# Performance work log

Measured on AMD Instinct MI355X. Metric: run time of the kernel, lower is better.

## Reference

```python
import jax, jax.numpy as jnp
import numpy as np

B, LA, LQ, LO, H, OUT = 32, 2048, 64, 32, 1024, 5


def _kaiming(key, out_f, in_f):
    return jax.random.normal(key, (out_f, in_f), jnp.float32) * np.sqrt(2.0 / in_f)


def setup_inputs() -> dict:
    key = jax.random.key(0)
    ks = jax.random.split(key, 16)
    inp = {
        "article_contexts": jax.random.normal(ks[0], (B, LA, H), jnp.float32),
        "question_contexts": jax.random.normal(ks[1], (B, LQ, H), jnp.float32),
        "options_embeds": jax.random.normal(ks[2], (B, 5, LO, H), jnp.float32),
        "answer_indices": jax.random.randint(ks[3], (B,), 0, LQ),
    }
    # mlp_att (article-question attention) params
    inp["a_Qw"], inp["a_Qb"] = _kaiming(ks[4], H, H), jnp.zeros((H,), jnp.float32)
    inp["a_Kw"], inp["a_Kb"] = _kaiming(ks[5], H, H), jnp.zeros((H,), jnp.float32)
    inp["a_Vw"], inp["a_Vb"] = _kaiming(ks[6], H, H), jnp.zeros((H,), jnp.float32)
    inp["a_vw"], inp["a_vb"] = _kaiming(ks[7], 1, H), jnp.zeros((1,), jnp.float32)
    # dot_layer (option attention) params
    inp["d_Qw"], inp["d_Qb"] = _kaiming(ks[8], H, H), jnp.zeros((H,), jnp.float32)
    inp["d_Kw"], inp["d_Kb"] = _kaiming(ks[9], H, H), jnp.zeros((H,), jnp.float32)
    inp["d_Vw"], inp["d_Vb"] = _kaiming(ks[10], H, H), jnp.zeros((H,), jnp.float32)
    inp["d_vw"], inp["d_vb"] = _kaiming(ks[11], 1, H), jnp.zeros((1,), jnp.float32)
    # final linear: hidden_size*5 -> output_dim
    inp["f_w"], inp["f_b"] = _kaiming(ks[12], OUT, 5 * H), jnp.zeros((OUT,), jnp.float32)
    return inp


def _mlp_att(Q, K, V, Qw, Qb, Kw, Kb, Vw, Vb, vw, vb):
    # Q: [B, H]; K, V: [B, (..opt..), L, H]. Dropout is identity (eval mode).
    Qp = Q @ Qw.T + Qb                      # [B, H]
    Kp = K @ Kw.T + Kb                      # [..., L, H]
    Vp = V @ Vw.T + Vb                      # [..., L, H]
    while Qp.ndim < Kp.ndim:
        Qp = Qp[..., None, :]
    M = jnp.tanh(Qp + Kp)                   # [..., L, H]
    scores = jax.nn.softmax(M @ vw.T + vb, axis=-2)  # softmax over L, [..., L, 1]
    return jnp.sum(Vp * scores, axis=-2)    # [..., H]


def reference(article_contexts, question_contexts, options_embeds, answer_indices,
              a_Qw, a_Qb, a_Kw, a_Kb, a_Vw, a_Vb, a_vw, a_vb,
              d_Qw, d_Qb, d_Kw, d_Kb, d_Vw, d_Vb, d_vw, d_vb,
              f_w, f_b):
    b = article_contexts.shape[0]
    # gather question context at the answer index -> [B, H]
    oqc = question_contexts[jnp.arange(b), answer_indices]
    # article-question additive attention -> [B, H]
    aq = _mlp_att(oqc, article_contexts, article_contexts,
                  a_Qw, a_Qb, a_Kw, a_Kb, a_Vw, a_Vb, a_vw, a_vb)
    # per-option additive attention, vectorized over the 5 options -> [B, 5, H]
    feats = _mlp_att(aq, options_embeds, options_embeds,
                     d_Qw, d_Qb, d_Kw, d_Kb, d_Vw, d_Vb, d_vw, d_vb)
    # concat options along feature dim, final linear -> [B, OUT]
    logits = feats.reshape(b, -1) @ f_w.T + f_b
    return logits
```

## Files before the change

### kernel.cpp

```cpp
#include <hip/hip_runtime.h>
#include <hip/hip_bf16.h>
#include <math.h>

#define HDIM 1024
#define NB 32
#define LA 2048
#define LO 32

typedef __attribute__((ext_vector_type(8))) short bf16x8;
typedef __attribute__((ext_vector_type(4))) float f32x4;
typedef unsigned int u32;

__device__ __forceinline__ float tanh_fast(float x){
    return 2.0f / (1.0f + __expf(-2.0f * x)) - 1.0f;
}

__device__ __forceinline__ void load_lds16(const void* gptr, void* lptr){
    __builtin_amdgcn_global_load_lds(
        (const __attribute__((address_space(1))) u32*)gptr,
        (__attribute__((address_space(3))) u32*)lptr, 16, 0, 0);
}

__global__ void zero_kernel(float* __restrict__ p, int n){
    int i = blockIdx.x * blockDim.x + threadIdx.x;
    int stride = gridDim.x * blockDim.x;
    for (; i < n; i += stride) p[i] = 0.0f;
}

__global__ void conv_bf16_kernel(const float* __restrict__ in, __hip_bfloat16* __restrict__ out, long n){
    long i = ((long)blockIdx.x * blockDim.x + threadIdx.x) * 4;
    long stride = (long)gridDim.x * blockDim.x * 4;
    for (; i < n; i += stride){
        float4 v = *(const float4*)(in + i);
        union { __hip_bfloat16 h[4]; short4 s; } u;
        u.h[0] = __float2bfloat16(v.x); u.h[1] = __float2bfloat16(v.y);
        u.h[2] = __float2bfloat16(v.z); u.h[3] = __float2bfloat16(v.w);
        *(short4*)(out + i) = u.s;
    }
}

__global__ void gather_kernel(const float* __restrict__ qc, const int* __restrict__ ans,
                              float* __restrict__ oqc){
    int b = blockIdx.x, tid = threadIdx.x;
    int idx = ans[b];
    const float* src = qc + ((size_t)b * 64 + idx) * HDIM;
    float* dst = oqc + (size_t)b * HDIM;
    #pragma unroll
    for (int l = 0; l < 4; l++) dst[tid + l * 256] = src[tid + l * 256];
}

__global__ __launch_bounds__(256) void proj_kernel(
    const float* __restrict__ in, const float* __restrict__ W,
    const float* __restrict__ bias, float* __restrict__ out){
    __shared__ float xin[HDIM];
    const int g = blockIdx.x, tid = threadIdx.x;
    const int lane = tid & 63, wave = tid >> 6;
    *(float4*)&xin[tid * 4] = *(const float4*)&in[(size_t)g * HDIM + tid * 4];
    __syncthreads();
    float4 xv[4];
    #pragma unroll
    for (int c = 0; c < 4; c++) xv[c] = *(const float4*)&xin[(c * 64 + lane) * 4];
    const int hbase = blockIdx.y * 64 + wave * 16;
    #pragma unroll 4
    for (int r = 0; r < 16; r++){
        int h = hbase + r;
        const float* Wr = W + (size_t)h * HDIM;
        float p = 0.f;
        #pragma unroll
        for (int c = 0; c < 4; c++){
            float4 wv = *(const float4*)&Wr[(c * 64 + lane) * 4];
            p = fmaf(xv[c].x, wv.x, p); p = fmaf(xv[c].y, wv.y, p);
            p = fmaf(xv[c].z, wv.z, p); p = fmaf(xv[c].w, wv.w, p);
        }
        #pragma unroll
        for (int off = 1; off < 64; off <<= 1) p += __shfl_xor(p, off, 64);
        if (lane == 0) out[(size_t)g * HDIM + h] = p + bias[h];
    }
}

__global__ __launch_bounds__(512, 2) void score_mfma8p(
    const __hip_bfloat16* __restrict__ X, const __hip_bfloat16* __restrict__ Kw,
    const float* __restrict__ Kb, const float* __restrict__ Qp,
    const float* __restrict__ vw, float* __restrict__ s,
    int row_off, int rows_per_batch)
{
    __shared__ __align__(16) char lds[131072];
    const int tid = threadIdx.x;
    const int lane = tid & 63, wid = tid >> 6;
    const int wm = wid >> 2, wn = wid & 3;
    const int lr = lane & 15, lg = lane >> 4;

    const int na = gridDim.x >> 2;
    const int bid = blockIdx.x;
    const int xcd = bid & 7, seq = bid >> 3;
    const int a_idx = xcd * (na >> 3) + (seq >> 2);
    const int h_idx = seq & 3;
    const int a0 = a_idx * 256, h0 = h_idx * 256;

    f32x4 acc[8][4] = {};
    bf16x8 av[8], bv[4];

    const int rA = tid >> 2;
    const int csw = ((tid & 3) * 16) ^ (((rA >> 1) & 3) << 4);
    const char* pA = (const char*)Kw + (size_t)(h0 + rA) * 2048 + csw;
    const char* pB = (const char*)X  + (size_t)(a0 + rA) * 2048 + csw;
    char* dst0 = lds + tid * 16;

    int aoff[8], boff[4];
    #pragma unroll
    for (int hf = 0; hf < 8; hf++){
        int rw = wm * 128 + hf * 16 + lr;
        aoff[hf] = rw * 64 + ((lg * 16) ^ (((rw >> 1) & 3) << 4));
    }
    #pragma unroll
    for (int af = 0; af < 4; af++){
        int rw = wn * 64 + af * 16 + lr;
        boff[af] = 16384 + rw * 64 + ((lg * 16) ^ (((rw >> 1) & 3) << 4));
    }

#define ISSUE(P, KOFF, SLOT, PLANE) do { \
    load_lds16((P) + (KOFF), dst0 + (SLOT) + (PLANE)); \
    load_lds16((P) + (KOFF) + 262144, dst0 + (SLOT) + (PLANE) + 8192); } while(0)
#define READS_A(BASE) do { \
    _Pragma("unroll") \
    for (int hf = 0; hf < 8; hf++) av[hf] = *(const bf16x8*)(lds + (BASE) + aoff[hf]); \
    bv[0] = *(const bf16x8*)(lds + (BASE) + boff[0]); \
    bv[1] = *(const bf16x8*)(lds + (BASE) + boff[1]); } while(0)
#define READS_B(BASE) do { \
    bv[2] = *(const bf16x8*)(lds + (BASE) + boff[2]); \
    bv[3] = *(const bf16x8*)(lds + (BASE) + boff[3]); } while(0)
#define MFMA2(A0, A1) do { __builtin_amdgcn_s_setprio(1); \
    _Pragma("unroll") \
    for (int hf = 0; hf < 8; hf++){ \
        acc[hf][A0] = __builtin_amdgcn_mfma_f32_16x16x32_bf16(av[hf], bv[A0], acc[hf][A0], 0, 0, 0); \
        acc[hf][A1] = __builtin_amdgcn_mfma_f32_16x16x32_bf16(av[hf], bv[A1], acc[hf][A1], 0, 0, 0); } \
    __builtin_amdgcn_s_setprio(0); } while(0)
#define BAR() __builtin_amdgcn_s_barrier()

    ISSUE(pA, 0, 0, 0);        ISSUE(pB, 0, 0, 16384);
    ISSUE(pA, 64, 0, 32768);   ISSUE(pB, 64, 0, 49152);
    ISSUE(pA, 128, 65536, 0);  ISSUE(pB, 128, 65536, 16384);

    for (int t = 0; t < 14; ++t){
        const int st = (t & 1) << 16;
        const int so = st ^ 65536;
        const int kb = t * 128;
        ISSUE(pA, kb + 192, so, 32768);
        asm volatile("s_waitcnt vmcnt(10)" ::: "memory");
        BAR();
        READS_A(st);
        BAR();
        MFMA2(0, 1);
        ISSUE(pB, kb + 192, so, 49152);
        READS_B(st);
        BAR();
        MFMA2(2, 3);
        ISSUE(pA, kb + 256, st, 0);
        asm volatile("s_waitcnt vmcnt(10)" ::: "memory");
        BAR();
        READS_A(st + 32768);
        BAR();
        MFMA2(0, 1);
        ISSUE(pB, kb + 256, st, 16384);
        READS_B(st + 32768);
        BAR();
        MFMA2(2, 3);
    }
    {
        ISSUE(pA, 14 * 128 + 192, 65536, 32768);
        asm volatile("s_waitcnt vmcnt(10)" ::: "memory");
        BAR(); READS_A(0); BAR(); MFMA2(0, 1);
        ISSUE(pB, 14 * 128 + 192, 65536, 49152);
        READS_B(0); BAR(); MFMA2(2, 3);
        asm volatile("s_waitcnt vmcnt(8)" ::: "memory");
        BAR(); READS_A(32768); BAR(); MFMA2(0, 1);
        READS_B(32768); BAR(); MFMA2(2, 3);
    }
    {
        asm volatile("s_waitcnt vmcnt(4)" ::: "memory");
        BAR(); READS_A(65536); BAR(); MFMA2(0, 1);
        READS_B(65536); BAR(); MFMA2(2, 3);
        asm volatile("s_waitcnt vmcnt(0)" ::: "memory");
        BAR(); READS_A(65536 + 32768); BAR(); MFMA2(0, 1);
        READS_B(65536 + 32768); BAR(); MFMA2(2, 3);
    }

    const int b = (row_off + a0) / rows_per_batch;
    float part[4] = {0.f, 0.f, 0.f, 0.f};
    #pragma unroll
    for (int hf = 0; hf < 8; hf++){
        int hbase = h0 + wm * 128 + hf * 16 + lg * 4;
        float4 kb4 = *(const float4*)(Kb + hbase);
        float4 qp4 = *(const float4*)(Qp + (size_t)b * HDIM + hbase);
        float4 vw4 = *(const float4*)(vw + hbase);
        float q0v = kb4.x + qp4.x, q1v = kb4.y + qp4.y;
        float q2v = kb4.z + qp4.z, q3v = kb4.w + qp4.w;
        #pragma unroll
        for (int af = 0; af < 4; af++){
            part[af] += tanh_fast(acc[hf][af][0] + q0v) * vw4.x;
            part[af] += tanh_fast(acc[hf][af][1] + q1v) * vw4.y;
            part[af] += tanh_fast(acc[hf][af][2] + q2v) * vw4.z;
            part[af] += tanh_fast(acc[hf][af][3] + q3v) * vw4.w;
        }
    }
    #pragma unroll
    for (int af = 0; af < 4; af++){
        float p = part[af];
        p += __shfl_xor(p, 16, 64);
        p += __shfl_xor(p, 32, 64);
        if (lane < 16)
            atomicAdd(&s[row_off + a0 + wn * 64 + af * 16 + lr], p);
    }
#undef ISSUE
#undef READS_A
#undef READS_B
#undef MFMA2
#undef BAR
}

#define SBM 128
#define SBN 128
__global__ __launch_bounds__(256) void score_mfma_kernel(
    const __hip_bfloat16* __restrict__ X, const __hip_bfloat16* __restrict__ Kw,
    const float* __restrict__ Kb, const float* __restrict__ Qp,
    const float* __restrict__ vw, float* __restrict__ s,
    int row_off, int rows_per_batch)
{
    __shared__ __align__(16) __hip_bfloat16 As[SBM][32];
    __shared__ __align__(16) __hip_bfloat16 Bs[SBN][32];
    const int tid = threadIdx.x;
    const int lane = tid & 63, wid = tid >> 6;
    const int wm = wid >> 1, wn = wid & 1;
    const int row0 = blockIdx.x * SBM;
    const int h0 = blockIdx.y * SBN;
    const int lr = lane & 15, lg = lane >> 4;

    f32x4 acc[4][4] = {};

    for (int k0 = 0; k0 < HDIM; k0 += 32){
        #pragma unroll
        for (int l = 0; l < 2; l++){
            int f = tid + l * 256;
            int r = f >> 2, c8 = (f & 3) * 8;
            load_lds16(X + (size_t)(row0 + r) * HDIM + k0 + c8, &As[0][0] + f * 8);
            load_lds16(Kw + (size_t)(h0 + r) * HDIM + k0 + c8, &Bs[0][0] + f * 8);
        }
        __syncthreads();
        bf16x8 a[4], b[4];
        #pragma unroll
        for (int i = 0; i < 4; i++)
            a[i] = *(const bf16x8*)&As[wm * 64 + i * 16 + lr][lg * 8];
        #pragma unroll
        for (int j = 0; j < 4; j++)
            b[j] = *(const bf16x8*)&Bs[wn * 64 + j * 16 + lr][lg * 8];
        #pragma unroll
        for (int i = 0; i < 4; i++)
            #pragma unroll
            for (int j = 0; j < 4; j++)
                acc[i][j] = __builtin_amdgcn_mfma_f32_16x16x32_bf16(a[i], b[j], acc[i][j], 0, 0, 0);
        __syncthreads();
    }

    float kbv[4], vwv[4];
    #pragma unroll
    for (int j = 0; j < 4; j++){
        int h = h0 + wn * 64 + j * 16 + lr;
        kbv[j] = Kb[h]; vwv[j] = vw[h];
    }
    #pragma unroll
    for (int i = 0; i < 4; i++){
        #pragma unroll
        for (int reg = 0; reg < 4; reg++){
            int r = row0 + wm * 64 + i * 16 + lg * 4 + reg;
            int gr = row_off + r;
            int bb = gr / rows_per_batch;
            const float* Qpb = Qp + (size_t)bb * HDIM;
            float p = 0.f;
            #pragma unroll
            for (int j = 0; j < 4; j++){
                int h = h0 + wn * 64 + j * 16 + lr;
                p += tanh_fast(acc[i][j][reg] + kbv[j] + Qpb[h]) * vwv[j];
            }
            #pragma unroll
            for (int off = 1; off < 16; off <<= 1) p += __shfl_xor(p, off, 16);
            if (lr == 0) atomicAdd(&s[gr], p);
        }
    }
}

__global__ void softmax_kernel(float* __restrict__ s, int Rg){
    __shared__ float red[4];
    int g = blockIdx.x, tid = threadIdx.x;
    float* sg = s + (size_t)g * Rg;
    float m = -INFINITY;
    for (int i = tid; i < Rg; i += 256) m = fmaxf(m, sg[i]);
    #pragma unroll
    for (int off = 32; off > 0; off >>= 1) m = fmaxf(m, __shfl_down(m, off, 64));
    if ((tid & 63) == 0) red[tid >> 6] = m;
    __syncthreads();
    m = fmaxf(fmaxf(red[0], red[1]), fmaxf(red[2], red[3]));
    __syncthreads();
    float sum = 0.f;
    for (int i = tid; i < Rg; i += 256){ float e = __expf(sg[i] - m); sg[i] = e; sum += e; }
    #pragma unroll
    for (int off = 32; off > 0; off >>= 1) sum += __shfl_down(sum, off, 64);
    if ((tid & 63) == 0) red[tid >> 6] = sum;
    __syncthreads();
    float inv = 1.0f / (red[0] + red[1] + red[2] + red[3]);
    for (int i = tid; i < Rg; i += 256) sg[i] *= inv;
}

__global__ void wsum_kernel(const float* __restrict__ X, const float* __restrict__ sc,
                            float* __restrict__ out, int Rg, int rowsPerChunk){
    __shared__ float scs[256];
    int g = blockIdx.x >> 2;
    int kc = blockIdx.x & 3;
    int i0 = blockIdx.y * rowsPerChunk;
    int tid = threadIdx.x;
    if (tid < rowsPerChunk) scs[tid] = sc[(size_t)g * Rg + i0 + tid];
    __syncthreads();
    int k = kc * 256 + tid;
    const float* Xg = X + ((size_t)g * Rg + i0) * HDIM + k;
    float acc = 0.f;
    for (int i = 0; i < rowsPerChunk; i++)
        acc += scs[i] * Xg[(size_t)i * HDIM];
    atomicAdd(&out[(size_t)g * HDIM + k], acc);
}

__global__ void wsum_bf16_kernel(const __hip_bfloat16* __restrict__ X, const float* __restrict__ sc,
                                 float* __restrict__ out, int Rg, int rowsPerChunk){
    __shared__ float scs[256];
    int g = blockIdx.x >> 2;
    int kc = blockIdx.x & 3;
    int i0 = blockIdx.y * rowsPerChunk;
    int tid = threadIdx.x;
    if (tid < rowsPerChunk) scs[tid] = sc[(size_t)g * Rg + i0 + tid];
    __syncthreads();
    int k = kc * 256 + tid;
    const __hip_bfloat16* Xg = X + ((size_t)g * Rg + i0) * HDIM + k;
    float acc = 0.f;
    for (int i = 0; i < rowsPerChunk; i++)
        acc += scs[i] * __bfloat162float(Xg[(size_t)i * HDIM]);
    atomicAdd(&out[(size_t)g * HDIM + k], acc);
}

__global__ void final_kernel(const float* __restrict__ feats, const float* __restrict__ fw,
                             const float* __restrict__ fb, float* __restrict__ out){
    __shared__ float red[4];
    int b = blockIdx.x, tid = threadIdx.x;
    const float* fe = feats + (size_t)b * 5120;
    for (int j = 0; j < 5; j++){
        float acc = 0.f;
        for (int i = tid; i < 5120; i += 256) acc += fe[i] * fw[(size_t)j * 5120 + i];
        #pragma unroll
        for (int off = 32; off > 0; off >>= 1) acc += __shfl_down(acc, off, 64);
        if ((tid & 63) == 0) red[tid >> 6] = acc;
        __syncthreads();
        if (tid == 0) out[b * 5 + j] = fb[j] + red[0] + red[1] + red[2] + red[3];
        __syncthreads();
    }
}

extern "C" void kernel_launch(void* const* d_in, const int* in_sizes, int n_in,
                              void* d_out, int out_size, void* d_ws, size_t ws_size,
                              hipStream_t stream) {
    const float* article  = (const float*)d_in[0];
    const float* question = (const float*)d_in[1];
    const float* options  = (const float*)d_in[2];
    const int*   ans      = (const int*)d_in[3];
    const float* a_Qw = (const float*)d_in[4];  const float* a_Qb = (const float*)d_in[5];
    const float* a_Kw = (const float*)d_in[6];  const float* a_Kb = (const float*)d_in[7];
    const float* a_Vw = (const float*)d_in[8];  const float* a_Vb = (const float*)d_in[9];
    const float* a_vw = (const float*)d_in[10];
    const float* d_Qw = (const float*)d_in[12]; const float* d_Qb = (const float*)d_in[13];
    const float* d_Kw = (const float*)d_in[14]; const float* d_Kb = (const float*)d_in[15];
    const float* d_Vw = (const float*)d_in[16]; const float* d_Vb = (const float*)d_in[17];
    const float* d_vw = (const float*)d_in[18];
    const float* f_w  = (const float*)d_in[20]; const float* f_b  = (const float*)d_in[21];
    float* out = (float*)d_out;

    float* ws = (float*)d_ws;
    float* oqc   = ws;
    float* qp_a  = ws + 32768;
    float* aq    = ws + 65536;
    float* qp_d  = ws + 98304;
    float* feats = ws + 131072;
    float* s_art = ws + 294912;
    float* s_opt = ws + 360448;
    float* w_art = ws + 365568;
    float* wd    = ws + 398336;
    __hip_bfloat16* kwa_bf = (__hip_bfloat16*)(ws + 562176);
    __hip_bfloat16* kwd_bf = kwa_bf + 1048576;
    __hip_bfloat16* opt_bf = kwd_bf + 1048576;
    __hip_bfloat16* art_bf = opt_bf + 5242880;
    size_t used_bytes = 562176 * 4 + (size_t)(1048576 * 2 + 5242880) * 2;
    long avail_rows = (long)((ws_size - used_bytes) / (HDIM * 2));
    int rows_total = NB * LA;
    int chunk_rows = (int)(avail_rows < rows_total ? avail_rows : rows_total);
    chunk_rows &= ~2047;
    if (chunk_rows < 2048) chunk_rows = 2048;

    zero_kernel<<<256, 256, 0, stream>>>(s_art, 267264);
    gather_kernel<<<NB, 256, 0, stream>>>(question, ans, oqc);
    proj_kernel<<<dim3(NB, 16), 256, 0, stream>>>(oqc, a_Qw, a_Qb, qp_a);
    conv_bf16_kernel<<<64, 256, 0, stream>>>(a_Kw, kwa_bf, 1048576);

    for (int r0 = 0; r0 < rows_total; r0 += chunk_rows){
        int nr = rows_total - r0; if (nr > chunk_rows) nr = chunk_rows;
        conv_bf16_kernel<<<1024, 256, 0, stream>>>(article + (size_t)r0 * HDIM, art_bf, (long)nr * HDIM);
        score_mfma8p<<<(nr / 256) * 4, 512, 0, stream>>>(
            art_bf, kwa_bf, a_Kb, qp_a, a_vw, s_art, r0, LA);
    }
    softmax_kernel<<<NB, 256, 0, stream>>>(s_art, LA);
    if (chunk_rows >= rows_total)
        wsum_bf16_kernel<<<dim3(NB * 4, 8), 256, 0, stream>>>(art_bf, s_art, w_art, LA, 256);
    else
        wsum_kernel<<<dim3(NB * 4, 8), 256, 0, stream>>>(article, s_art, w_art, LA, 256);
    proj_kernel<<<dim3(NB, 16), 256, 0, stream>>>(w_art, a_Vw, a_Vb, aq);

    proj_kernel<<<dim3(NB, 16), 256, 0, stream>>>(aq, d_Qw, d_Qb, qp_d);
    conv_bf16_kernel<<<64, 256, 0, stream>>>(d_Kw, kwd_bf, 1048576);
    conv_bf16_kernel<<<320, 256, 0, stream>>>(options, opt_bf, 5242880);
    score_mfma_kernel<<<dim3((NB * 5 * LO) / SBM, HDIM / SBN), 256, 0, stream>>>(
        opt_bf, kwd_bf, d_Kb, qp_d, d_vw, s_opt, 0, 5 * LO);
    softmax_kernel<<<NB * 5, 256, 0, stream>>>(s_opt, LO);
    wsum_kernel<<<dim3(NB * 5 * 4, 1), 256, 0, stream>>>(options, s_opt, wd, LO, LO);
    proj_kernel<<<dim3(NB * 5, 16), 256, 0, stream>>>(wd, d_Vw, d_Vb, feats);
    final_kernel<<<NB, 256, 0, stream>>>(feats, f_w, f_b, out);
}
```

Before: 439.4 us.

## Fuse gather into projection, merge conversions, vectorize weighted sums, drop chunking

Folds the answer-index gather into the query projection kernel and merges the two option-side bf16 conversions into a single launch. The article and option weighted-sum kernels now read bf16 data with short4 vector loads, one block per batch slice. The option path reads bf16 options instead of fp32. Workspace-based chunking of the article path is removed and the score kernel is launched once, so a workspace at least the size of the full bf16 article copy is now assumed. The zeroed region is shrunk to match.

```diff
diff --git a/kernel.cpp b/kernel.cpp
--- a/kernel.cpp
+++ b/kernel.cpp
@@ -39,14 +39,60 @@
     }
 }
 
-__global__ void gather_kernel(const float* __restrict__ qc, const int* __restrict__ ans,
-                              float* __restrict__ oqc){
-    int b = blockIdx.x, tid = threadIdx.x;
-    int idx = ans[b];
-    const float* src = qc + ((size_t)b * 64 + idx) * HDIM;
-    float* dst = oqc + (size_t)b * HDIM;
-    #pragma unroll
-    for (int l = 0; l < 4; l++) dst[tid + l * 256] = src[tid + l * 256];
+__global__ void conv2_bf16_kernel(const float* __restrict__ in0, __hip_bfloat16* __restrict__ out0, long n0,
+                                  const float* __restrict__ in1, __hip_bfloat16* __restrict__ out1, long n1){
+    const float* in; __hip_bfloat16* out; long n; long base;
+    if (blockIdx.x < 64){ in = in0; out = out0; n = n0; base = (long)blockIdx.x; 
+        long i = (base * blockDim.x + threadIdx.x) * 4;
+        long stride = 64L * blockDim.x * 4;
+        for (; i < n; i += stride){
+            float4 v = *(const float4*)(in + i);
+            union { __hip_bfloat16 h[4]; short4 s; } u;
+            u.h[0] = __float2bfloat16(v.x); u.h[1] = __float2bfloat16(v.y);
+            u.h[2] = __float2bfloat16(v.z); u.h[3] = __float2bfloat16(v.w);
+            *(short4*)(out + i) = u.s;
+        }
+    } else { in = in1; out = out1; n = n1; base = (long)(blockIdx.x - 64);
+        long i = (base * blockDim.x + threadIdx.x) * 4;
+        long stride = 320L * blockDim.x * 4;
+        for (; i < n; i += stride){
+            float4 v = *(const float4*)(in + i);
+            union { __hip_bfloat16 h[4]; short4 s; } u;
+            u.h[0] = __float2bfloat16(v.x); u.h[1] = __float2bfloat16(v.y);
+            u.h[2] = __float2bfloat16(v.z); u.h[3] = __float2bfloat16(v.w);
+            *(short4*)(out + i) = u.s;
+        }
+    }
+}
+
+__global__ __launch_bounds__(256) void proj_q_kernel(
+    const float* __restrict__ question, const int* __restrict__ ans,
+    const float* __restrict__ W, const float* __restrict__ bias, float* __restrict__ out){
+    __shared__ float xin[HDIM];
+    const int g = blockIdx.x, tid = threadIdx.x;
+    const int lane = tid & 63, wave = tid >> 6;
+    const float* in = question + ((size_t)g * 64 + ans[g]) * HDIM;
+    *(float4*)&xin[tid * 4] = *(const float4*)&in[tid * 4];
+    __syncthreads();
+    float4 xv[4];
+    #pragma unroll
+    for (int c = 0; c < 4; c++) xv[c] = *(const float4*)&xin[(c * 64 + lane) * 4];
+    const int hbase = blockIdx.y * 64 + wave * 16;
+    #pragma unroll 4
+    for (int r = 0; r < 16; r++){
+        int h = hbase + r;
+        const float* Wr = W + (size_t)h * HDIM;
+        float p = 0.f;
+        #pragma unroll
+        for (int c = 0; c < 4; c++){
+            float4 wv = *(const float4*)&Wr[(c * 64 + lane) * 4];
+            p = fmaf(xv[c].x, wv.x, p); p = fmaf(xv[c].y, wv.y, p);
+            p = fmaf(xv[c].z, wv.z, p); p = fmaf(xv[c].w, wv.w, p);
+        }
+        #pragma unroll
+        for (int off = 1; off < 64; off <<= 1) p += __shfl_xor(p, off, 64);
+        if (lane == 0) out[(size_t)g * HDIM + h] = p + bias[h];
+    }
 }
 
 __global__ __launch_bounds__(256) void proj_kernel(
@@ -78,11 +124,12 @@
     }
 }
 
+#define NTT 16
 __global__ __launch_bounds__(512, 2) void score_mfma8p(
     const __hip_bfloat16* __restrict__ X, const __hip_bfloat16* __restrict__ Kw,
     const float* __restrict__ Kb, const float* __restrict__ Qp,
     const float* __restrict__ vw, float* __restrict__ s,
-    int row_off, int rows_per_batch)
+    int rows_per_batch)
 {
     __shared__ __align__(16) char lds[131072];
     const int tid = threadIdx.x;
@@ -185,7 +232,7 @@
         READS_B(65536 + 32768); BAR(); MFMA2(2, 3);
     }
 
-    const int b = (row_off + a0) / rows_per_batch;
+    const int b = a0 / rows_per_batch;
     float part[4] = {0.f, 0.f, 0.f, 0.f};
     #pragma unroll
     for (int hf = 0; hf < 8; hf++){
@@ -209,7 +256,7 @@
         p += __shfl_xor(p, 16, 64);
         p += __shfl_xor(p, 32, 64);
         if (lane < 16)
-            atomicAdd(&s[row_off + a0 + wn * 64 + af * 16 + lr], p);
+            atomicAdd(&s[a0 + wn * 64 + af * 16 + lr], p);
     }
 #undef ISSUE
 #undef READS_A
@@ -310,38 +357,47 @@
     for (int i = tid; i < Rg; i += 256) sg[i] *= inv;
 }
 
-__global__ void wsum_kernel(const float* __restrict__ X, const float* __restrict__ sc,
-                            float* __restrict__ out, int Rg, int rowsPerChunk){
+__global__ __launch_bounds__(256) void wsum_art_v(
+    const __hip_bfloat16* __restrict__ X, const float* __restrict__ sc,
+    float* __restrict__ out){
     __shared__ float scs[256];
-    int g = blockIdx.x >> 2;
-    int kc = blockIdx.x & 3;
-    int i0 = blockIdx.y * rowsPerChunk;
-    int tid = threadIdx.x;
-    if (tid < rowsPerChunk) scs[tid] = sc[(size_t)g * Rg + i0 + tid];
-    __syncthreads();
-    int k = kc * 256 + tid;
-    const float* Xg = X + ((size_t)g * Rg + i0) * HDIM + k;
-    float acc = 0.f;
-    for (int i = 0; i < rowsPerChunk; i++)
-        acc += scs[i] * Xg[(size_t)i * HDIM];
-    atomicAdd(&out[(size_t)g * HDIM + k], acc);
-}
-
-__global__ void wsum_bf16_kernel(const __hip_bfloat16* __restrict__ X, const float* __restrict__ sc,
-                                 float* __restrict__ out, int Rg, int rowsPerChunk){
-    __shared__ float scs[256];
-    int g = blockIdx.x >> 2;
-    int kc = blockIdx.x & 3;
-    int i0 = blockIdx.y * rowsPerChunk;
-    int tid = threadIdx.x;
-    if (tid < rowsPerChunk) scs[tid] = sc[(size_t)g * Rg + i0 + tid];
-    __syncthreads();
-    int k = kc * 256 + tid;
-    const __hip_bfloat16* Xg = X + ((size_t)g * Rg + i0) * HDIM + k;
-    float acc = 0.f;
-    for (int i = 0; i < rowsPerChunk; i++)
-        acc += scs[i] * __bfloat162float(Xg[(size_t)i * HDIM]);
-    atomicAdd(&out[(size_t)g * HDIM + k], acc);
+    const int g = blockIdx.x, ic = blockIdx.y, tid = threadIdx.x;
+    scs[tid] = sc[(size_t)g * LA + ic * 256 + tid];
+    __syncthreads();
+    const __hip_bfloat16* Xg = X + ((size_t)g * LA + ic * 256) * HDIM + tid * 4;
+    float a0 = 0.f, a1 = 0.f, a2 = 0.f, a3 = 0.f;
+    for (int i = 0; i < 256; i++){
+        short4 v = *(const short4*)(Xg + (size_t)i * HDIM);
+        float w = scs[i];
+        a0 = fmaf(w, __bfloat162float(*(const __hip_bfloat16*)&v.x), a0);
+        a1 = fmaf(w, __bfloat162float(*(const __hip_bfloat16*)&v.y), a1);
+        a2 = fmaf(w, __bfloat162float(*(const __hip_bfloat16*)&v.z), a2);
+        a3 = fmaf(w, __bfloat162float(*(const __hip_bfloat16*)&v.w), a3);
+    }
+    float* o = out + (size_t)g * HDIM + tid * 4;
+    atomicAdd(o + 0, a0); atomicAdd(o + 1, a1);
+    atomicAdd(o + 2, a2); atomicAdd(o + 3, a3);
+}
+
+__global__ __launch_bounds__(256) void wsum_opt_v(
+    const __hip_bfloat16* __restrict__ X, const float* __restrict__ sc,
+    float* __restrict__ out){
+    __shared__ float scs[LO];
+    const int g = blockIdx.x, tid = threadIdx.x;
+    if (tid < LO) scs[tid] = sc[(size_t)g * LO + tid];
+    __syncthreads();
+    const __hip_bfloat16* Xg = X + (size_t)g * LO * HDIM + tid * 4;
+    float a0 = 0.f, a1 = 0.f, a2 = 0.f, a3 = 0.f;
+    for (int i = 0; i < LO; i++){
+        short4 v = *(const short4*)(Xg + (size_t)i * HDIM);
+        float w = scs[i];
+        a0 = fmaf(w, __bfloat162float(*(const __hip_bfloat16*)&v.x), a0);
+        a1 = fmaf(w, __bfloat162float(*(const __hip_bfloat16*)&v.y), a1);
+        a2 = fmaf(w, __bfloat162float(*(const __hip_bfloat16*)&v.z), a2);
+        a3 = fmaf(w, __bfloat162float(*(const __hip_bfloat16*)&v.w), a3);
+    }
+    float* o = out + (size_t)g * HDIM + tid * 4;
+    o[0] = a0; o[1] = a1; o[2] = a2; o[3] = a3;
 }
 
 __global__ void final_kernel(const float* __restrict__ feats, const float* __restrict__ fw,
@@ -380,7 +436,6 @@
     float* out = (float*)d_out;
 
     float* ws = (float*)d_ws;
-    float* oqc   = ws;
     float* qp_a  = ws + 32768;
     float* aq    = ws + 65536;
     float* qp_d  = ws + 98304;
@@ -393,38 +448,25 @@
     __hip_bfloat16* kwd_bf = kwa_bf + 1048576;
     __hip_bfloat16* opt_bf = kwd_bf + 1048576;
     __hip_bfloat16* art_bf = opt_bf + 5242880;
-    size_t used_bytes = 562176 * 4 + (size_t)(1048576 * 2 + 5242880) * 2;
-    long avail_rows = (long)((ws_size - used_bytes) / (HDIM * 2));
-    int rows_total = NB * LA;
-    int chunk_rows = (int)(avail_rows < rows_total ? avail_rows : rows_total);
-    chunk_rows &= ~2047;
-    if (chunk_rows < 2048) chunk_rows = 2048;
-
-    zero_kernel<<<256, 256, 0, stream>>>(s_art, 267264);
-    gather_kernel<<<NB, 256, 0, stream>>>(question, ans, oqc);
-    proj_kernel<<<dim3(NB, 16), 256, 0, stream>>>(oqc, a_Qw, a_Qb, qp_a);
+
+    zero_kernel<<<128, 256, 0, stream>>>(s_art, 103424);
+    proj_q_kernel<<<dim3(NB, 16), 256, 0, stream>>>(question, ans, a_Qw, a_Qb, qp_a);
     conv_bf16_kernel<<<64, 256, 0, stream>>>(a_Kw, kwa_bf, 1048576);
-
-    for (int r0 = 0; r0 < rows_total; r0 += chunk_rows){
-        int nr = rows_total - r0; if (nr > chunk_rows) nr = chunk_rows;
-        conv_bf16_kernel<<<1024, 256, 0, stream>>>(article + (size_t)r0 * HDIM, art_bf, (long)nr * HDIM);
-        score_mfma8p<<<(nr / 256) * 4, 512, 0, stream>>>(
-            art_bf, kwa_bf, a_Kb, qp_a, a_vw, s_art, r0, LA);
-    }
+    conv_bf16_kernel<<<1024, 256, 0, stream>>>(article, art_bf, (long)NB * LA * HDIM);
+
+    score_mfma8p<<<(NB * LA / 256) * 4, 512, 0, stream>>>(
+        art_bf, kwa_bf, a_Kb, qp_a, a_vw, s_art, LA);
     softmax_kernel<<<NB, 256, 0, stream>>>(s_art, LA);
-    if (chunk_rows >= rows_total)
-        wsum_bf16_kernel<<<dim3(NB * 4, 8), 256, 0, stream>>>(art_bf, s_art, w_art, LA, 256);
-    else
-        wsum_kernel<<<dim3(NB * 4, 8), 256, 0, stream>>>(article, s_art, w_art, LA, 256);
+    wsum_art_v<<<dim3(NB, 8), 256, 0, stream>>>(art_bf, s_art, w_art);
     proj_kernel<<<dim3(NB, 16), 256, 0, stream>>>(w_art, a_Vw, a_Vb, aq);
 
     proj_kernel<<<dim3(NB, 16), 256, 0, stream>>>(aq, d_Qw, d_Qb, qp_d);
-    conv_bf16_kernel<<<64, 256, 0, stream>>>(d_Kw, kwd_bf, 1048576);
-    conv_bf16_kernel<<<320, 256, 0, stream>>>(options, opt_bf, 5242880);
+    conv2_bf16_kernel<<<384, 256, 0, stream>>>(d_Kw, kwd_bf, 1048576,
+                                               options, opt_bf, 5242880);
     score_mfma_kernel<<<dim3((NB * 5 * LO) / SBM, HDIM / SBN), 256, 0, stream>>>(
         opt_bf, kwd_bf, d_Kb, qp_d, d_vw, s_opt, 0, 5 * LO);
     softmax_kernel<<<NB * 5, 256, 0, stream>>>(s_opt, LO);
-    wsum_kernel<<<dim3(NB * 5 * 4, 1), 256, 0, stream>>>(options, s_opt, wd, LO, LO);
+    wsum_opt_v<<<NB * 5, 256, 0, stream>>>(opt_bf, s_opt, wd);
     proj_kernel<<<dim3(NB * 5, 16), 256, 0, stream>>>(wd, d_Vw, d_Vb, feats);
     final_kernel<<<NB, 256, 0, stream>>>(feats, f_w, f_b, out);
 }
```

After: 425.5 us. 1.03x faster.
